# Kernel tuning notes

Measured on AMD Instinct MI355X. Metric: run time of the kernel, lower is better.

The kernel has to match this reference:

```python
import jax, jax.numpy as jnp
import numpy as np

B, S, D = 2, 4096, 512
H = 8
HD = D // H


def setup_inputs() -> dict:
    key = jax.random.key(0)
    k1, k2, k3, k4, k5 = jax.random.split(key, 5)
    sd = 1.0 / np.sqrt(D)
    return {
        "x": jax.random.normal(k1, (B, S, D), dtype=jnp.float32),
        "Wqkv": jax.random.normal(k2, (3 * D, D), dtype=jnp.float32) * sd,
        "bqkv": jax.random.normal(k3, (3 * D,), dtype=jnp.float32) * 0.02,
        "Wo": jax.random.normal(k4, (D, D), dtype=jnp.float32) * sd,
        "bo": jax.random.normal(k5, (D,), dtype=jnp.float32) * 0.02,
    }


def reference(x, Wqkv, bqkv, Wo, bo):
    b, s, d = x.shape
    h, hd = H, d // H
    # QKV projection (torch Linear: x @ W^T + b)
    qkv = x @ Wqkv.T + bqkv                      # [b, s, 3d]
    q, k, v = jnp.split(qkv, 3, axis=-1)         # each [b, s, d]
    # [b, s, h, hd] -> [b, h, s, hd]
    q = q.reshape(b, s, h, hd).transpose(0, 2, 1, 3)
    k = k.reshape(b, s, h, hd).transpose(0, 2, 1, 3)
    v = v.reshape(b, s, h, hd).transpose(0, 2, 1, 3)
    # causal additive mask: triu(ones, diag=1) * -1e10
    mask = jnp.triu(jnp.ones((s, s), dtype=x.dtype), k=1) * jnp.asarray(-1e10, x.dtype)
    wts = jnp.einsum("bhqd,bhkd->bhqk", q, k) / np.sqrt(hd).astype(np.float32)
    wts = wts + mask[None, None, :, :]
    wts = jax.nn.softmax(wts, axis=-1)
    y = jnp.einsum("bhqk,bhkd->bhqd", wts, v)    # [b, h, s, hd]
    y = y.transpose(0, 2, 1, 3).reshape(b, s, d) # [b, s, d]
    out = y @ Wo.T + bo
    return out
```

## Files before the change

### kernel.cpp

```cpp
#include <hip/hip_runtime.h>


typedef __bf16 bf16x8 __attribute__((ext_vector_type(8)));
typedef float f32x4 __attribute__((ext_vector_type(4)));
typedef unsigned short u16;

#define MFMA(a, b, c) __builtin_amdgcn_mfma_f32_16x16x32_bf16(a, b, c, 0, 0, 0)
#define QSCALE 0.18033688011112042f
#define FIXEDM 12.0f

__device__ __forceinline__ float exp2_fast(float x) {
    return __builtin_amdgcn_exp2f(x);
}
__device__ __forceinline__ u16 f2bf(float f) {
    union { __bf16 h; u16 u; } v; v.h = (__bf16)f; return v.u;
}
__device__ __forceinline__ ushort4 f4_to_bf4(float4 v) {
    ushort4 r;
    r.x = f2bf(v.x); r.y = f2bf(v.y); r.z = f2bf(v.z); r.w = f2bf(v.w);
    return r;
}
__device__ __forceinline__ void load_lds16(const u16* g, u16* l) {
    __builtin_amdgcn_global_load_lds(
        (const __attribute__((address_space(1))) void*)g,
        (__attribute__((address_space(3))) void*)l, 16, 0, 0);
}

__global__ __launch_bounds__(256) void cvt_all(
    const float* __restrict__ x, const float* __restrict__ wq,
    const float* __restrict__ wo,
    u16* __restrict__ xb, u16* __restrict__ wqb, u16* __restrict__ wob)
{
    int i = blockIdx.x * 256 + threadIdx.x;
    if (i < 1048576) {
        ((ushort4*)xb)[i] = f4_to_bf4(((const float4*)x)[i]);
    } else if (i < 1048576 + 196608) {
        int j = i - 1048576;
        ((ushort4*)wqb)[j] = f4_to_bf4(((const float4*)wq)[j]);
    } else {
        int j = i - 1048576 - 196608;
        ((ushort4*)wob)[j] = f4_to_bf4(((const float4*)wo)[j]);
    }
}

__global__ __launch_bounds__(256) void gemm_qkv_bf(
    const u16* __restrict__ X, const u16* __restrict__ W,
    const float* __restrict__ bias,
    u16* __restrict__ QY, u16* __restrict__ Ko, u16* __restrict__ Vto)
{
    __shared__ u16 As[128 * 32];
    __shared__ u16 Bs[128 * 32];
    const int K = 512;
    const int tid = threadIdx.x, wave = tid >> 6, lane = tid & 63;
    const int l15 = lane & 15, quad = lane >> 4;
    const int bm = blockIdx.x * 128, bn = blockIdx.y * 128;
    const int wr = wave >> 1, wc = wave & 1;
    const int arow = lane >> 2;
    const int acol = (lane & 3) * 8;

    f32x4 acc[4][4] = {};
    for (int k0 = 0; k0 < K; k0 += 32) {
        __syncthreads();
#pragma unroll
        for (int ii = 0; ii < 2; ii++) {
            const int inst = wave * 2 + ii;
            const int row = inst * 16 + arow;
            load_lds16(&X[(bm + row) * K + k0 + acol], &As[inst * 512]);
            load_lds16(&W[(bn + row) * K + k0 + acol], &Bs[inst * 512]);
        }
        __syncthreads();
        bf16x8 a[4], b[4];
#pragma unroll
        for (int i = 0; i < 4; i++)
            a[i] = *(const bf16x8*)&As[(wr * 64 + i * 16 + l15) * 32 + quad * 8];
#pragma unroll
        for (int j = 0; j < 4; j++)
            b[j] = *(const bf16x8*)&Bs[(wc * 64 + j * 16 + l15) * 32 + quad * 8];
#pragma unroll
        for (int i = 0; i < 4; i++)
#pragma unroll
            for (int j = 0; j < 4; j++)
                acc[i][j] = MFMA(b[i], a[j], acc[i][j]);
    }

    const int nbase = bn + wc * 64;
    const int which = nbase >> 9;
#pragma unroll
    for (int i = 0; i < 4; i++) {
        const int d0 = nbase + i * 16 + quad * 4;
        const float4 bv = *(const float4*)&bias[d0];
        const int d0m = d0 & 511;
        const int h = d0m >> 6, hd0 = d0m & 63;
#pragma unroll
        for (int j = 0; j < 4; j++) {
            const int s_g = bm + wr * 64 + j * 16 + l15;
            const int b_ = s_g >> 12, s0 = s_g & 4095;
            const int bhh = b_ * 8 + h;
            if (which == 2) {
#pragma unroll
                for (int r = 0; r < 4; r++) {
                    const float bvr = (r == 0) ? bv.x : (r == 1) ? bv.y : (r == 2) ? bv.z : bv.w;
                    Vto[((size_t)(bhh * 64 + hd0 + r)) * 4096 + s0] = f2bf(acc[i][j][r] + bvr);
                }
            } else if (which == 1) {
                ushort4 pk;
                pk.x = f2bf(acc[i][j][0] + bv.x);
                pk.y = f2bf(acc[i][j][1] + bv.y);
                pk.z = f2bf(acc[i][j][2] + bv.z);
                pk.w = f2bf(acc[i][j][3] + bv.w);
                *(ushort4*)&Ko[(bhh * 4096 + s0) * 64 + hd0] = pk;
            } else {
                ushort4 pk;
                pk.x = f2bf((acc[i][j][0] + bv.x) * QSCALE);
                pk.y = f2bf((acc[i][j][1] + bv.y) * QSCALE);
                pk.z = f2bf((acc[i][j][2] + bv.z) * QSCALE);
                pk.w = f2bf((acc[i][j][3] + bv.w) * QSCALE);
                *(ushort4*)&QY[((b_ * 4096 + s0) * 8 + h) * 64 + hd0] = pk;
            }
        }
    }
}

#define LS 72

__global__ __launch_bounds__(256, 4) void attn_k(
    const u16* __restrict__ QY, const u16* __restrict__ Kk, const u16* __restrict__ Vt,
    u16* __restrict__ PO, float* __restrict__ ML)
{
    __shared__ u16 Ks[64 * 64];
    __shared__ u16 Vs[64 * 64];
    __shared__ u16 Ps[4 * 16 * LS];

    const int tid = threadIdx.x, wave = tid >> 6, lane = tid & 63;
    const int l15 = lane & 15, quad = lane >> 4;
    const int bh = blockIdx.x;
    const int b_ = bh >> 3, h = bh & 7;
    const int u = (int)blockIdx.y;
    const int layer = u >> 4;
    const int p = u & 15;
    const int pp = p >> 1, seg = p & 1;
    const int qt = layer * 8 + ((layer & 1) ? (7 - pp) : pp);
    const int kt0 = seg ? (qt + 1) : 0;
    const int kt1 = seg ? (2 * qt + 2) : (qt + 1);
    const int base_r = qt * 128 + wave * 32;

    const u16* qpa = &QY[((b_ * 4096 + base_r + l15) * 8 + h) * 64];
    const u16* qpb = qpa + 16 * 8 * 64;
    bf16x8 qa0 = *(const bf16x8*)&qpa[quad * 8];
    bf16x8 qa1 = *(const bf16x8*)&qpa[32 + quad * 8];
    bf16x8 qb0 = *(const bf16x8*)&qpb[quad * 8];
    bf16x8 qb1 = *(const bf16x8*)&qpb[32 + quad * 8];

    f32x4 oa[4] = {}, ob[4] = {};
    f32x4 lacc_a = {}, lacc_b = {};

    const int r0 = tid >> 3;
    const int swz = 8 * ((tid & 7) ^ (r0 & 7));
    const u16* KgA = &Kk[(size_t)bh * 4096 * 64 + r0 * 64 + swz];
    const u16* VgA = &Vt[(size_t)bh * 64 * 4096 + r0 * 4096 + swz];
    u16* ldsK0 = &Ks[wave * 512];
    u16* ldsK1 = &Ks[wave * 512 + 2048];
    u16* ldsV0 = &Vs[wave * 512];
    u16* ldsV1 = &Vs[wave * 512 + 2048];

    const int c0 = 8 * (quad ^ (l15 & 7));

    bf16x8 ones;
#pragma unroll
    for (int i = 0; i < 8; i++) ones[i] = (__bf16)1.0f;

    u16* P = &Ps[wave * 16 * LS];

    for (int kt = kt0; kt < kt1; kt++) {
        const int k0 = kt * 64;
        __syncthreads();
        load_lds16(KgA + kt * 4096, ldsK0);
        load_lds16(KgA + kt * 4096 + 2048, ldsK1);
        load_lds16(VgA + k0, ldsV0);
        load_lds16(VgA + k0 + 131072, ldsV1);
        __syncthreads();

        f32x4 sa[4], sb[4];
#pragma unroll
        for (int j = 0; j < 4; j++) {
            const int kb = (j * 16 + l15) * 64;
            bf16x8 kf0 = *(const bf16x8*)&Ks[kb + c0];
            bf16x8 kf1 = *(const bf16x8*)&Ks[kb + (c0 ^ 32)];
            f32x4 s = {};
            s = MFMA(kf0, qa0, s);
            s = MFMA(kf1, qa1, s);
            sa[j] = s;
            f32x4 t = {};
            t = MFMA(kf0, qb0, t);
            t = MFMA(kf1, qb1, t);
            sb[j] = t;
        }

        {
            const bool needmask = (k0 + 63 > base_r);
            float spa[4][4];
#pragma unroll
            for (int j = 0; j < 4; j++)
#pragma unroll
                for (int r = 0; r < 4; r++) {
                    float v = sa[j][r];
                    if (needmask) {
                        const int key = k0 + j * 16 + quad * 4 + r;
                        if (key > base_r + l15) v = -1e30f;
                    }
                    spa[j][r] = exp2_fast(v - FIXEDM);
                }
#pragma unroll
            for (int j = 0; j < 4; j++) {
                ushort4 w;
                w.x = f2bf(spa[j][0]); w.y = f2bf(spa[j][1]);
                w.z = f2bf(spa[j][2]); w.w = f2bf(spa[j][3]);
                *(ushort4*)&P[l15 * LS + j * 16 + quad * 4] = w;
            }
        }

        float spb[4][4];
        {
            const bool needmask = (k0 + 63 > base_r + 16);
#pragma unroll
            for (int j = 0; j < 4; j++)
#pragma unroll
                for (int r = 0; r < 4; r++) {
                    float v = sb[j][r];
                    if (needmask) {
                        const int key = k0 + j * 16 + quad * 4 + r;
                        if (key > base_r + 16 + l15) v = -1e30f;
                    }
                    spb[j][r] = exp2_fast(v - FIXEDM);
                }
        }

        bf16x8 pfa0 = *(const bf16x8*)&P[l15 * LS + quad * 8];
        bf16x8 pfa1 = *(const bf16x8*)&P[l15 * LS + 32 + quad * 8];
#pragma unroll
        for (int j = 0; j < 4; j++) {
            ushort4 w;
            w.x = f2bf(spb[j][0]); w.y = f2bf(spb[j][1]);
            w.z = f2bf(spb[j][2]); w.w = f2bf(spb[j][3]);
            *(ushort4*)&P[l15 * LS + j * 16 + quad * 4] = w;
        }
        bf16x8 pfb0 = *(const bf16x8*)&P[l15 * LS + quad * 8];
        bf16x8 pfb1 = *(const bf16x8*)&P[l15 * LS + 32 + quad * 8];

        lacc_a = MFMA(ones, pfa0, lacc_a);
        lacc_a = MFMA(ones, pfa1, lacc_a);
        lacc_b = MFMA(ones, pfb0, lacc_b);
        lacc_b = MFMA(ones, pfb1, lacc_b);

#pragma unroll
        for (int n = 0; n < 4; n++) {
            const int vb = (n * 16 + l15) * 64;
            bf16x8 vf0 = *(const bf16x8*)&Vs[vb + c0];
            bf16x8 vf1 = *(const bf16x8*)&Vs[vb + (c0 ^ 32)];
            oa[n] = MFMA(vf0, pfa0, oa[n]);
            oa[n] = MFMA(vf1, pfa1, oa[n]);
            ob[n] = MFMA(vf0, pfb0, ob[n]);
            ob[n] = MFMA(vf1, pfb1, ob[n]);
        }
    }

    const float lfa = lacc_a[0];
    const float lfb = lacc_b[0];
    const float iva = (lfa > 0.0f) ? 1.0f / lfa : 0.0f;
    const float ivb = (lfb > 0.0f) ? 1.0f / lfb : 0.0f;
    u16* ppa = &PO[(size_t)seg * 4194304 +
                   (size_t)((b_ * 4096 + base_r + l15) * 8 + h) * 64];
    u16* ppb = ppa + 16 * 8 * 64;
#pragma unroll
    for (int n = 0; n < 4; n++) {
        ushort4 wa;
        wa.x = f2bf(oa[n][0] * iva);
        wa.y = f2bf(oa[n][1] * iva);
        wa.z = f2bf(oa[n][2] * iva);
        wa.w = f2bf(oa[n][3] * iva);
        *(ushort4*)&ppa[n * 16 + quad * 4] = wa;
        ushort4 wb;
        wb.x = f2bf(ob[n][0] * ivb);
        wb.y = f2bf(ob[n][1] * ivb);
        wb.z = f2bf(ob[n][2] * ivb);
        wb.w = f2bf(ob[n][3] * ivb);
        *(ushort4*)&ppb[n * 16 + quad * 4] = wb;
    }
    if (quad == 0) {
        float* mpa = &ML[((seg * 16 + bh) * 4096 + base_r + l15) * 2];
        mpa[0] = FIXEDM;
        mpa[1] = lfa;
        float* mpb = mpa + 16 * 2;
        mpb[0] = FIXEDM;
        mpb[1] = lfb;
    }
}

__global__ __launch_bounds__(256) void merge_k(
    const u16* __restrict__ PO, const float* __restrict__ ML, u16* __restrict__ Y)
{
    const int flat = blockIdx.x * 256 + threadIdx.x;
    const int rs = flat >> 6;
    const int rem = flat & 63;
    const int h = rem >> 3, c = rem & 7;
    const int b_ = rs >> 12, s = rs & 4095;
    const int bh = b_ * 8 + h;
    const float m0 = ML[(bh * 4096 + s) * 2];
    const float l0 = ML[(bh * 4096 + s) * 2 + 1];
    const float m1 = ML[((16 + bh) * 4096 + s) * 2];
    const float l1 = ML[((16 + bh) * 4096 + s) * 2 + 1];
    const float m = fmaxf(m0, m1);
    const float w0 = (l0 > 0.0f) ? exp2_fast(m0 - m) * l0 : 0.0f;
    const float w1 = (l1 > 0.0f) ? exp2_fast(m1 - m) * l1 : 0.0f;
    const float inv = 1.0f / (w0 + w1);
    const float a0 = w0 * inv, a1 = w1 * inv;

    const size_t base = (size_t)(rs * 8 + h) * 64 + c * 8;
    bf16x8 x0 = *(const bf16x8*)&PO[base];
    bf16x8 x1 = *(const bf16x8*)&PO[4194304 + base];
    ushort4 lo, hi;
    lo.x = f2bf(a0 * (float)x0[0] + a1 * (float)x1[0]);
    lo.y = f2bf(a0 * (float)x0[1] + a1 * (float)x1[1]);
    lo.z = f2bf(a0 * (float)x0[2] + a1 * (float)x1[2]);
    lo.w = f2bf(a0 * (float)x0[3] + a1 * (float)x1[3]);
    hi.x = f2bf(a0 * (float)x0[4] + a1 * (float)x1[4]);
    hi.y = f2bf(a0 * (float)x0[5] + a1 * (float)x1[5]);
    hi.z = f2bf(a0 * (float)x0[6] + a1 * (float)x1[6]);
    hi.w = f2bf(a0 * (float)x0[7] + a1 * (float)x1[7]);
    *(ushort4*)&Y[base] = lo;
    *(ushort4*)&Y[base + 4] = hi;
}

__global__ __launch_bounds__(256) void gemm_o_bf(
    const u16* __restrict__ X, const u16* __restrict__ W,
    const float* __restrict__ bias, float* __restrict__ Out)
{
    __shared__ u16 As[128 * 32];
    __shared__ u16 Bs[128 * 32];
    const int K = 512;
    const int tid = threadIdx.x, wave = tid >> 6, lane = tid & 63;
    const int l15 = lane & 15, quad = lane >> 4;
    const int bm = blockIdx.x * 128, bn = blockIdx.y * 128;
    const int wr = wave >> 1, wc = wave & 1;
    const int arow = lane >> 2;
    const int acol = (lane & 3) * 8;

    f32x4 acc[4][4] = {};
    for (int k0 = 0; k0 < K; k0 += 32) {
        __syncthreads();
#pragma unroll
        for (int ii = 0; ii < 2; ii++) {
            const int inst = wave * 2 + ii;
            const int row = inst * 16 + arow;
            load_lds16(&X[(bm + row) * K + k0 + acol], &As[inst * 512]);
            load_lds16(&W[(bn + row) * K + k0 + acol], &Bs[inst * 512]);
        }
        __syncthreads();
        bf16x8 a[4], b[4];
#pragma unroll
        for (int i = 0; i < 4; i++)
            a[i] = *(const bf16x8*)&As[(wr * 64 + i * 16 + l15) * 32 + quad * 8];
#pragma unroll
        for (int j = 0; j < 4; j++)
            b[j] = *(const bf16x8*)&Bs[(wc * 64 + j * 16 + l15) * 32 + quad * 8];
#pragma unroll
        for (int i = 0; i < 4; i++)
#pragma unroll
            for (int j = 0; j < 4; j++)
                acc[i][j] = MFMA(b[i], a[j], acc[i][j]);
    }
#pragma unroll
    for (int i = 0; i < 4; i++) {
        const int n0 = bn + wc * 64 + i * 16 + quad * 4;
        const float4 bv = *(const float4*)&bias[n0];
#pragma unroll
        for (int j = 0; j < 4; j++) {
            const int m = bm + wr * 64 + j * 16 + l15;
            float4 ov;
            ov.x = acc[i][j][0] + bv.x;
            ov.y = acc[i][j][1] + bv.y;
            ov.z = acc[i][j][2] + bv.z;
            ov.w = acc[i][j][3] + bv.w;
            *(float4*)&Out[(size_t)m * 512 + n0] = ov;
        }
    }
}

extern "C" void kernel_launch(void* const* d_in, const int* in_sizes, int n_in,
                              void* d_out, int out_size, void* d_ws, size_t ws_size,
                              hipStream_t stream) {
    (void)in_sizes; (void)n_in; (void)out_size; (void)ws_size;
    const float* x    = (const float*)d_in[0];
    const float* Wqkv = (const float*)d_in[1];
    const float* bqkv = (const float*)d_in[2];
    const float* Wo   = (const float*)d_in[3];
    const float* bo   = (const float*)d_in[4];
    float* out = (float*)d_out;

    u16* qy_ws = (u16*)d_ws;
    u16* k_ws  = qy_ws + 4194304;
    u16* vt_ws = k_ws + 4194304;
    float* ml  = (float*)(vt_ws + 4194304);
    u16* wqkvb = (u16*)(ml + 262144);
    u16* wob   = wqkvb + 786432;
    u16* xb    = (u16*)d_out;
    u16* po    = (u16*)d_out;

    cvt_all<<<5120, 256, 0, stream>>>(x, Wqkv, Wo, xb, wqkvb, wob);
    gemm_qkv_bf<<<dim3(64, 12), 256, 0, stream>>>(xb, wqkvb, bqkv, qy_ws, k_ws, vt_ws);
    attn_k<<<dim3(16, 64), 256, 0, stream>>>(qy_ws, k_ws, vt_ws, po, ml);
    merge_k<<<2048, 256, 0, stream>>>(po, ml, qy_ws);
    gemm_o_bf<<<dim3(64, 4), 256, 0, stream>>>(qy_ws, wob, bo, out);
}
```

Before: 195.2 us.

## Double-buffer LDS tiles in GEMMs and attention; fold mask offset into MFMA init

Both GEMM kernels and the attention kernel now keep two LDS buffers and prefetch the next K-tile with async global-to-LDS loads while the current tile is computed. Raw s_barrier and hand-written vmcnt waits replace __syncthreads. In attention, the V tile load is overlapped with the QK^T and softmax phase, and the causal mask plus fixed max offset are folded into the MFMA accumulator init instead of applied after. The aim is to hide global load latency and cut VALU work, at the cost of more LDS per block (which may limit occupancy) and fragile manual vmcnt counting.

```diff
diff --git a/kernel.cpp b/kernel.cpp
--- a/kernel.cpp
+++ b/kernel.cpp
@@ -48,8 +48,8 @@
     const float* __restrict__ bias,
     u16* __restrict__ QY, u16* __restrict__ Ko, u16* __restrict__ Vto)
 {
-    __shared__ u16 As[128 * 32];
-    __shared__ u16 Bs[128 * 32];
+    __shared__ u16 As[2 * 128 * 32];
+    __shared__ u16 Bs[2 * 128 * 32];
     const int K = 512;
     const int tid = threadIdx.x, wave = tid >> 6, lane = tid & 63;
     const int l15 = lane & 15, quad = lane >> 4;
@@ -59,28 +59,44 @@
     const int acol = (lane & 3) * 8;
 
     f32x4 acc[4][4] = {};
+#pragma unroll
+    for (int ii = 0; ii < 2; ii++) {
+        const int inst = wave * 2 + ii;
+        const int row = inst * 16 + arow;
+        load_lds16(&X[(bm + row) * K + acol], &As[inst * 512]);
+        load_lds16(&W[(bn + row) * K + acol], &Bs[inst * 512]);
+    }
+    int cur = 0;
     for (int k0 = 0; k0 < K; k0 += 32) {
-        __syncthreads();
-#pragma unroll
-        for (int ii = 0; ii < 2; ii++) {
-            const int inst = wave * 2 + ii;
-            const int row = inst * 16 + arow;
-            load_lds16(&X[(bm + row) * K + k0 + acol], &As[inst * 512]);
-            load_lds16(&W[(bn + row) * K + k0 + acol], &Bs[inst * 512]);
-        }
-        __syncthreads();
+        __builtin_amdgcn_s_barrier();
+        if (k0 + 32 < K) {
+            const int nb = (cur ^ 1) * 4096;
+#pragma unroll
+            for (int ii = 0; ii < 2; ii++) {
+                const int inst = wave * 2 + ii;
+                const int row = inst * 16 + arow;
+                load_lds16(&X[(bm + row) * K + k0 + 32 + acol], &As[nb + inst * 512]);
+                load_lds16(&W[(bn + row) * K + k0 + 32 + acol], &Bs[nb + inst * 512]);
+            }
+            asm volatile("s_waitcnt vmcnt(4)" ::: "memory");
+        } else {
+            asm volatile("s_waitcnt vmcnt(0)" ::: "memory");
+        }
+        __builtin_amdgcn_s_barrier();
+        const int cb = cur * 4096;
         bf16x8 a[4], b[4];
 #pragma unroll
         for (int i = 0; i < 4; i++)
-            a[i] = *(const bf16x8*)&As[(wr * 64 + i * 16 + l15) * 32 + quad * 8];
+            a[i] = *(const bf16x8*)&As[cb + (wr * 64 + i * 16 + l15) * 32 + quad * 8];
 #pragma unroll
         for (int j = 0; j < 4; j++)
-            b[j] = *(const bf16x8*)&Bs[(wc * 64 + j * 16 + l15) * 32 + quad * 8];
+            b[j] = *(const bf16x8*)&Bs[cb + (wc * 64 + j * 16 + l15) * 32 + quad * 8];
 #pragma unroll
         for (int i = 0; i < 4; i++)
 #pragma unroll
             for (int j = 0; j < 4; j++)
                 acc[i][j] = MFMA(b[i], a[j], acc[i][j]);
+        cur ^= 1;
     }
 
     const int nbase = bn + wc * 64;
@@ -127,7 +143,7 @@
     const u16* __restrict__ QY, const u16* __restrict__ Kk, const u16* __restrict__ Vt,
     u16* __restrict__ PO, float* __restrict__ ML)
 {
-    __shared__ u16 Ks[64 * 64];
+    __shared__ u16 Ks[2 * 64 * 64];
     __shared__ u16 Vs[64 * 64];
     __shared__ u16 Ps[4 * 16 * LS];
 
@@ -158,10 +174,8 @@
     const int swz = 8 * ((tid & 7) ^ (r0 & 7));
     const u16* KgA = &Kk[(size_t)bh * 4096 * 64 + r0 * 64 + swz];
     const u16* VgA = &Vt[(size_t)bh * 64 * 4096 + r0 * 4096 + swz];
-    u16* ldsK0 = &Ks[wave * 512];
-    u16* ldsK1 = &Ks[wave * 512 + 2048];
-    u16* ldsV0 = &Vs[wave * 512];
-    u16* ldsV1 = &Vs[wave * 512 + 2048];
+    u16* Ksf = &Ks[0];
+    u16* Vsf = &Vs[0];
 
     const int c0 = 8 * (quad ^ (l15 & 7));
 
@@ -171,45 +185,67 @@
 
     u16* P = &Ps[wave * 16 * LS];
 
+    load_lds16(KgA + kt0 * 4096, Ksf + wave * 512);
+    load_lds16(KgA + kt0 * 4096 + 2048, Ksf + wave * 512 + 2048);
+
+    int cur = 0;
     for (int kt = kt0; kt < kt1; kt++) {
         const int k0 = kt * 64;
-        __syncthreads();
-        load_lds16(KgA + kt * 4096, ldsK0);
-        load_lds16(KgA + kt * 4096 + 2048, ldsK1);
-        load_lds16(VgA + k0, ldsV0);
-        load_lds16(VgA + k0 + 131072, ldsV1);
-        __syncthreads();
-
+        __builtin_amdgcn_s_barrier();
+        load_lds16(VgA + k0, Vsf + wave * 512);
+        load_lds16(VgA + k0 + 131072, Vsf + wave * 512 + 2048);
+        const bool havnext = (kt + 1 < kt1);
+        if (havnext) {
+            u16* kb = Ksf + (cur ^ 1) * 4096 + wave * 512;
+            load_lds16(KgA + (kt + 1) * 4096, kb);
+            load_lds16(KgA + (kt + 1) * 4096 + 2048, kb + 2048);
+            asm volatile("s_waitcnt vmcnt(4)" ::: "memory");
+        } else {
+            asm volatile("s_waitcnt vmcnt(2)" ::: "memory");
+        }
+        __builtin_amdgcn_s_barrier();
+
+        const u16* Kcur = Ksf + cur * 4096;
+        const bool nmA = (k0 + 63 > base_r);
+        const bool nmB = (k0 + 63 > base_r + 16);
         f32x4 sa[4], sb[4];
 #pragma unroll
         for (int j = 0; j < 4; j++) {
+            f32x4 ia, ib;
+            if (nmA) {
+#pragma unroll
+                for (int r = 0; r < 4; r++) {
+                    const int key = k0 + j * 16 + quad * 4 + r;
+                    ia[r] = (key > base_r + l15) ? -1e30f : -FIXEDM;
+                }
+            } else {
+                ia[0] = -FIXEDM; ia[1] = -FIXEDM; ia[2] = -FIXEDM; ia[3] = -FIXEDM;
+            }
+            if (nmB) {
+#pragma unroll
+                for (int r = 0; r < 4; r++) {
+                    const int key = k0 + j * 16 + quad * 4 + r;
+                    ib[r] = (key > base_r + 16 + l15) ? -1e30f : -FIXEDM;
+                }
+            } else {
+                ib[0] = -FIXEDM; ib[1] = -FIXEDM; ib[2] = -FIXEDM; ib[3] = -FIXEDM;
+            }
             const int kb = (j * 16 + l15) * 64;
-            bf16x8 kf0 = *(const bf16x8*)&Ks[kb + c0];
-            bf16x8 kf1 = *(const bf16x8*)&Ks[kb + (c0 ^ 32)];
-            f32x4 s = {};
-            s = MFMA(kf0, qa0, s);
-            s = MFMA(kf1, qa1, s);
-            sa[j] = s;
-            f32x4 t = {};
-            t = MFMA(kf0, qb0, t);
-            t = MFMA(kf1, qb1, t);
-            sb[j] = t;
+            bf16x8 kf0 = *(const bf16x8*)&Kcur[kb + c0];
+            bf16x8 kf1 = *(const bf16x8*)&Kcur[kb + (c0 ^ 32)];
+            ia = MFMA(kf0, qa0, ia);
+            sa[j] = MFMA(kf1, qa1, ia);
+            ib = MFMA(kf0, qb0, ib);
+            sb[j] = MFMA(kf1, qb1, ib);
         }
 
         {
-            const bool needmask = (k0 + 63 > base_r);
             float spa[4][4];
 #pragma unroll
             for (int j = 0; j < 4; j++)
 #pragma unroll
-                for (int r = 0; r < 4; r++) {
-                    float v = sa[j][r];
-                    if (needmask) {
-                        const int key = k0 + j * 16 + quad * 4 + r;
-                        if (key > base_r + l15) v = -1e30f;
-                    }
-                    spa[j][r] = exp2_fast(v - FIXEDM);
-                }
+                for (int r = 0; r < 4; r++)
+                    spa[j][r] = exp2_fast(sa[j][r]);
 #pragma unroll
             for (int j = 0; j < 4; j++) {
                 ushort4 w;
@@ -220,20 +256,11 @@
         }
 
         float spb[4][4];
-        {
-            const bool needmask = (k0 + 63 > base_r + 16);
-#pragma unroll
-            for (int j = 0; j < 4; j++)
-#pragma unroll
-                for (int r = 0; r < 4; r++) {
-                    float v = sb[j][r];
-                    if (needmask) {
-                        const int key = k0 + j * 16 + quad * 4 + r;
-                        if (key > base_r + 16 + l15) v = -1e30f;
-                    }
-                    spb[j][r] = exp2_fast(v - FIXEDM);
-                }
-        }
+#pragma unroll
+        for (int j = 0; j < 4; j++)
+#pragma unroll
+            for (int r = 0; r < 4; r++)
+                spb[j][r] = exp2_fast(sb[j][r]);
 
         bf16x8 pfa0 = *(const bf16x8*)&P[l15 * LS + quad * 8];
         bf16x8 pfa1 = *(const bf16x8*)&P[l15 * LS + 32 + quad * 8];
@@ -251,6 +278,13 @@
         lacc_a = MFMA(ones, pfa1, lacc_a);
         lacc_b = MFMA(ones, pfb0, lacc_b);
         lacc_b = MFMA(ones, pfb1, lacc_b);
+
+        if (havnext) {
+            asm volatile("s_waitcnt vmcnt(2)" ::: "memory");
+        } else {
+            asm volatile("s_waitcnt vmcnt(0)" ::: "memory");
+        }
+        __builtin_amdgcn_s_barrier();
 
 #pragma unroll
         for (int n = 0; n < 4; n++) {
@@ -262,6 +296,7 @@
             ob[n] = MFMA(vf0, pfb0, ob[n]);
             ob[n] = MFMA(vf1, pfb1, ob[n]);
         }
+        cur ^= 1;
     }
 
     const float lfa = lacc_a[0];
@@ -335,8 +370,8 @@
     const u16* __restrict__ X, const u16* __restrict__ W,
     const float* __restrict__ bias, float* __restrict__ Out)
 {
-    __shared__ u16 As[128 * 32];
-    __shared__ u16 Bs[128 * 32];
+    __shared__ u16 As[2 * 128 * 32];
+    __shared__ u16 Bs[2 * 128 * 32];
     const int K = 512;
     const int tid = threadIdx.x, wave = tid >> 6, lane = tid & 63;
     const int l15 = lane & 15, quad = lane >> 4;
@@ -346,28 +381,44 @@
     const int acol = (lane & 3) * 8;
 
     f32x4 acc[4][4] = {};
+#pragma unroll
+    for (int ii = 0; ii < 2; ii++) {
+        const int inst = wave * 2 + ii;
+        const int row = inst * 16 + arow;
+        load_lds16(&X[(bm + row) * K + acol], &As[inst * 512]);
+        load_lds16(&W[(bn + row) * K + acol], &Bs[inst * 512]);
+    }
+    int cur = 0;
     for (int k0 = 0; k0 < K; k0 += 32) {
-        __syncthreads();
-#pragma unroll
-        for (int ii = 0; ii < 2; ii++) {
-            const int inst = wave * 2 + ii;
-            const int row = inst * 16 + arow;
-            load_lds16(&X[(bm + row) * K + k0 + acol], &As[inst * 512]);
-            load_lds16(&W[(bn + row) * K + k0 + acol], &Bs[inst * 512]);
-        }
-        __syncthreads();
+        __builtin_amdgcn_s_barrier();
+        if (k0 + 32 < K) {
+            const int nb = (cur ^ 1) * 4096;
+#pragma unroll
+            for (int ii = 0; ii < 2; ii++) {
+                const int inst = wave * 2 + ii;
+                const int row = inst * 16 + arow;
+                load_lds16(&X[(bm + row) * K + k0 + 32 + acol], &As[nb + inst * 512]);
+                load_lds16(&W[(bn + row) * K + k0 + 32 + acol], &Bs[nb + inst * 512]);
+            }
+            asm volatile("s_waitcnt vmcnt(4)" ::: "memory");
+        } else {
+            asm volatile("s_waitcnt vmcnt(0)" ::: "memory");
+        }
+        __builtin_amdgcn_s_barrier();
+        const int cb = cur * 4096;
         bf16x8 a[4], b[4];
 #pragma unroll
         for (int i = 0; i < 4; i++)
-            a[i] = *(const bf16x8*)&As[(wr * 64 + i * 16 + l15) * 32 + quad * 8];
+            a[i] = *(const bf16x8*)&As[cb + (wr * 64 + i * 16 + l15) * 32 + quad * 8];
 #pragma unroll
         for (int j = 0; j < 4; j++)
-            b[j] = *(const bf16x8*)&Bs[(wc * 64 + j * 16 + l15) * 32 + quad * 8];
+            b[j] = *(const bf16x8*)&Bs[cb + (wc * 64 + j * 16 + l15) * 32 + quad * 8];
 #pragma unroll
         for (int i = 0; i < 4; i++)
 #pragma unroll
             for (int j = 0; j < 4; j++)
                 acc[i][j] = MFMA(b[i], a[j], acc[i][j]);
+        cur ^= 1;
     }
 #pragma unroll
     for (int i = 0; i < 4; i++) {
```

Measured after the change: 182.5 us. 1.07x faster.
